# Kernel tuning notes

Hardware: AMD Instinct MI355X
Metric: run time of the kernel (lower is better)

## Reference

```python
import jax, jax.numpy as jnp
import numpy as np


def _gru_dir(x, Wih, Whh, bih, bhh):
    # x: (B,T,I) -> (B,T,H); torch GRU equations, h0 = 0
    H = Whh.shape[1]
    pre = x @ Wih.T + bih  # (B,T,3H), input projection hoisted out of scan
    def step(h, p):
        gh = h @ Whh.T + bhh
        pr, pz, pn = jnp.split(p, 3, axis=-1)
        gr, gz, gn = jnp.split(gh, 3, axis=-1)
        r = jax.nn.sigmoid(pr + gr)
        z = jax.nn.sigmoid(pz + gz)
        n = jnp.tanh(pn + r * gn)
        h = (1.0 - z) * n + z * h
        return h, h
    h0 = jnp.zeros((x.shape[0], H), x.dtype)
    _, ys = jax.lax.scan(step, h0, jnp.swapaxes(pre, 0, 1))
    return jnp.swapaxes(ys, 0, 1)


def _gru_bidir(x, Wih, Whh, bih, bhh):
    f = _gru_dir(x, Wih[0], Whh[0], bih[0], bhh[0])
    b = _gru_dir(x[:, ::-1], Wih[1], Whh[1], bih[1], bhh[1])[:, ::-1]
    return jnp.concatenate([f, b], axis=-1)


def _forward(inputs, embed, l_Wih, l_Whh, l_bih, l_bhh, r_Wih, r_Whh, r_bih, r_bhh,
             a_Wih, a_Whh, a_bih, a_bhh, Wc1, Wc2, vc, Wb, Wd, vd, Wm, vm, Ws, vs,
             Wp, vp, Wpred):
    x = embed[inputs]  # (B,T,E)
    hl = _gru_bidir(x, l_Wih, l_Whh, l_bih, l_bhh)  # (B,T,2H)
    hr = _gru_bidir(x, r_Wih, r_Whh, r_bih, r_bhh)  # (B,T,2H)
    # co-attention: score[b,i,j] = vc . tanh(Wc1 hl_j + Wc2 hr_i)
    s = jnp.tanh((hl @ Wc1.T)[:, None, :, :] + (hr @ Wc2.T)[:, :, None, :])  # (B,T,T,H)
    ptc = jax.nn.softmax((s @ vc.T)[..., 0], axis=-1) @ hl
    # bilinear: hr (Wb hl)^T
    sjt = jnp.einsum('bid,bjd->bij', hr, hl @ Wb.T)
    ptb = jax.nn.softmax(sjt, axis=-1) @ hl
    # multiplicative: vd . tanh(Wd (hl_j * hr_i))
    p = hl[:, None, :, :] * hr[:, :, None, :]  # (B,T,T,2H)
    ptd = jax.nn.softmax((jnp.tanh(p @ Wd.T) @ vd.T)[..., 0], axis=-1) @ hl
    # subtractive: vm . tanh(Wm (hl_j - hr_i))
    d = hl[:, None, :, :] - hr[:, :, None, :]  # (B,T,T,2H)
    ptm = jax.nn.softmax((jnp.tanh(d @ Wm.T) @ vm.T)[..., 0], axis=-1) @ hl
    # self-attention on hr: vs . tanh(Ws (hr_j * hr_i))
    ss = hr[:, None, :, :] * hr[:, :, None, :]  # (B,T,T,2H)
    pts = jax.nn.softmax((jnp.tanh(ss @ Ws.T) @ vs.T)[..., 0], axis=-1) @ hr
    agg = jnp.concatenate([hr, pts, ptc, ptd, ptb, ptm], axis=-1)  # (B,T,12H)
    ar = _gru_bidir(agg, a_Wih, a_Whh, a_bih, a_bhh)  # (B,T,2H)
    # pooling of hl
    sj = jax.nn.softmax(jnp.swapaxes(jnp.tanh(hl @ Wp.T) @ vp.T, 1, 2), axis=-1)  # (B,1,T)
    rl = sj @ hl  # (B,1,2H)
    # final attention over aggregation
    sj2 = jax.nn.softmax(jnp.swapaxes((ar @ Wc1.T + rl @ Wc2.T) @ vc.T, 1, 2), axis=-1)  # (B,1,T)
    rr = (sj2 @ ar)[:, 0, :]  # (B,2H)
    return jax.nn.sigmoid(rr @ Wpred.T)  # (B,labels)


def setup_inputs() -> dict:
    B, T, V, E, H, L = 4, 256, 30000, 300, 128, 2
    key = jax.random.key(0)
    ks = jax.random.split(key, 40)
    inp = {}
    inp['inputs'] = jax.random.randint(ks[0], (B, T), 0, V)
    inp['embed'] = jax.random.uniform(ks[1], (V, E), jnp.float32, -0.1, 0.1)
    ki = 2
    for name, isz in [('l', E), ('r', E), ('a', 12 * H)]:
        inp[name + '_Wih'] = jax.random.normal(ks[ki], (2, 3 * H, isz), jnp.float32) * 0.05; ki += 1
        inp[name + '_Whh'] = jax.random.normal(ks[ki], (2, 3 * H, H), jnp.float32) * 0.05; ki += 1
        inp[name + '_bih'] = jnp.zeros((2, 3 * H), jnp.float32)
        inp[name + '_bhh'] = jnp.zeros((2, 3 * H), jnp.float32)
    for n, o, i in [('Wc1', H, 2 * H), ('Wc2', H, 2 * H), ('vc', 1, H), ('Wb', 2 * H, 2 * H),
                    ('Wd', H, 2 * H), ('vd', 1, H), ('Wm', H, 2 * H), ('vm', 1, H),
                    ('Ws', H, 2 * H), ('vs', 1, H), ('Wp', H, 2 * H), ('vp', 1, H),
                    ('Wpred', L, 2 * H)]:
        inp[n] = jax.random.normal(ks[ki], (o, i), jnp.float32) * 0.05; ki += 1
    return inp


def reference(inputs, embed, l_Wih, l_Whh, l_bih, l_bhh, r_Wih, r_Whh, r_bih, r_bhh,
              a_Wih, a_Whh, a_bih, a_bhh, Wc1, Wc2, vc, Wb, Wd, vd, Wm, vm, Ws, vs,
              Wp, vp, Wpred):
    return _forward(inputs, embed, l_Wih, l_Whh, l_bih, l_bhh, r_Wih, r_Whh, r_bih,
                    r_bhh, a_Wih, a_Whh, a_bih, a_bhh, Wc1, Wc2, vc, Wb, Wd, vd, Wm,
                    vm, Ws, vs, Wp, vp, Wpred)
```

## Files before the change

### kernel.cpp

```cpp
#include <hip/hip_runtime.h>


#define DEV static __device__ __forceinline__
#define BAR_LGKM() __asm__ volatile("s_waitcnt lgkmcnt(0)\ns_barrier" ::: "memory")

typedef __attribute__((ext_vector_type(4))) float f32x4;
typedef __attribute__((ext_vector_type(8))) short s16x8;
typedef __attribute__((ext_vector_type(4))) unsigned int u32x4;
typedef __attribute__((ext_vector_type(2))) unsigned int u32x2;

constexpr int T = 256, E = 300, EP = 320, H = 128, H2 = 256, H3 = 384, H12 = 1536;
constexpr int M = 1024;
constexpr int STY = 262144;

DEV float b2f(unsigned short h) { return __uint_as_float(((unsigned)h) << 16); }
DEV unsigned short f2b(float f) {
  unsigned u = __float_as_uint(f);
  u += 0x7fff + ((u >> 16) & 1);
  return (unsigned short)(u >> 16);
}
DEV unsigned cvt_pk_bf16(float lo, float hi) {
  unsigned r;
  __asm__("v_cvt_pk_bf16_f32 %0, %1, %2" : "=v"(r) : "v"(lo), "v"(hi));
  return r;
}
DEV float rcp_f(float x) {
  float r;
  __asm__("v_rcp_f32 %0, %1" : "=v"(r) : "v"(x));
  return r;
}
DEV float sigm(float x) { return rcp_f(1.f + __expf(-x)); }
DEV float tanh_f(float x) {
  float e = __expf(2.f * x);
  return __builtin_fmaf(-2.f, rcp_f(e + 1.f), 1.f);
}
DEV float plsel(float x0, float x1) {
  u32x2 r = __builtin_amdgcn_permlane32_swap(
      __float_as_uint(x0), __float_as_uint(x1), false, false);
  return __uint_as_float(r[0]);
}

DEV s16x8 ldfrag(const unsigned short* p) {
  u32x4 v = *(const u32x4*)p;
  return __builtin_bit_cast(s16x8, v);
}
DEV f32x4 mfma16(s16x8 a, s16x8 b, f32x4 c) {
  return __builtin_amdgcn_mfma_f32_16x16x32_bf16(a, b, c, 0, 0, 0);
}


struct StageArgs {
  const float* cs[9]; unsigned short* cd[9]; int cn[9];
  const int* idx; const float* emb; unsigned short* xhi; unsigned short* xlo;
  const float* lW; const float* rW; unsigned short* wpad;
  int bo[12];
};

__global__ void k_stage(StageArgs sa) {
  int blk = blockIdx.x;
  int seg = 0;
  #pragma unroll
  for (int s2 = 1; s2 < 11; ++s2) seg = (blk >= sa.bo[s2]) ? s2 : seg;
  int i = (blk - sa.bo[seg]) * 256 + threadIdx.x;
  if (seg < 9) {
    if (i < sa.cn[seg]) sa.cd[seg][i] = f2b(sa.cs[seg][i]);
    return;
  }
  if (seg == 9) {
    if (i >= M * EP) return;
    int m = i / EP, e = i - m * EP;
    int r = sa.idx[m];
    float v = (e < E) ? sa.emb[(size_t)r * E + e] : 0.f;
    unsigned short hi = f2b(v);
    sa.xhi[i] = hi;
    sa.xlo[i] = f2b(v - b2f(hi));
    return;
  }
  if (i >= 4 * H3 * EP) return;
  int e = i % EP, n = (i / EP) % H3, uu = i / (EP * H3);
  const float* src = (uu < 2 ? sa.lW : sa.rW) + (size_t)((uu & 1) * H3 + n) * E;
  sa.wpad[i] = (e < E) ? f2b(src[e]) : (unsigned short)0;
}


struct GemmDesc {
  const unsigned short* Ahi; const unsigned short* Alo; const unsigned short* W;
  const float* bias; float* Cf; int N; int K; int tr;
};
struct GemmBatch { GemmDesc d[8]; };

DEV void gemm_body(const GemmDesc& g, int mb, int nb, int tid) {
  int lane = tid & 63, w = tid >> 6, quad = lane >> 4, l16 = lane & 15;
  int K = g.K;
  const unsigned short* Ahp = g.Ahi + (size_t)(mb + w * 16 + l16) * K + quad * 8;
  const unsigned short* Alp = g.Alo + (size_t)(mb + w * 16 + l16) * K + quad * 8;
  const unsigned short* Wp = g.W + (size_t)(nb + l16) * K + quad * 8;
  f32x4 acc[4];
  #pragma unroll
  for (int nt = 0; nt < 4; ++nt) acc[nt] = f32x4{0.f, 0.f, 0.f, 0.f};
  for (int k = 0; k < K; k += 32) {
    s16x8 ah = ldfrag(Ahp + k);
    s16x8 al = ldfrag(Alp + k);
    #pragma unroll
    for (int nt = 0; nt < 4; ++nt) {
      s16x8 b = ldfrag(Wp + (size_t)nt * 16 * K + k);
      acc[nt] = mfma16(ah, b, acc[nt]);
      acc[nt] = mfma16(al, b, acc[nt]);
    }
  }
  int mr0 = mb + w * 16 + quad * 4;
  #pragma unroll
  for (int nt = 0; nt < 4; ++nt) {
    int col = nb + nt * 16 + l16;
    float bv = g.bias ? g.bias[col] : 0.f;
    #pragma unroll
    for (int r = 0; r < 4; ++r) {
      if (g.tr)
        g.Cf[(size_t)col * M + (mr0 + r)] = acc[nt][r] + bv;
      else
        g.Cf[(size_t)(mr0 + r) * g.N + col] = acc[nt][r] + bv;
    }
  }
}

__global__ __launch_bounds__(256) void k_gemm(GemmBatch gb) {
  GemmDesc g = gb.d[blockIdx.z];
  int nb = blockIdx.y * 64;
  if (nb >= g.N) return;
  gemm_body(g, blockIdx.x * 64, nb, threadIdx.x);
}


struct RecArgs {
  const unsigned short* whh[4];
  const float* pre[4];
  float* outf[4];
  unsigned short* outhi[4];
  unsigned short* outlo[4];
  unsigned short* agghi[4];
  unsigned short* agglo[4];
  const float* bhh[4];
  int colOff[4];
  int dir[4];
};

#define GRU_STEP(pr_, pz_, pn_, pq_, hcur_, hnxt_)                             \
  {                                                                            \
    float pr = pr_, pz = pz_, pn = pn_;                                        \
    pq_ += pst2;                                                               \
    pr_ = pq_[0] + bh_r; pz_ = pq_[128] + bh_z; pn_ = pq_[256];                \
    const unsigned short* hb_ = hcur_ + l16 * 136 + quad * 8;                  \
    s16x8 ah0 = ldfrag(hb_);                                                   \
    s16x8 ah1 = ldfrag(hb_ + 32);                                              \
    s16x8 ah2 = ldfrag(hb_ + 64);                                              \
    s16x8 ah3 = ldfrag(hb_ + 96);                                              \
    f32x4 z4 = f32x4{0.f, 0.f, 0.f, 0.f};                                      \
    f32x4 aR0 = mfma16(ah0, bq[0][0], z4);                                     \
    f32x4 aR1 = mfma16(ah2, bq[0][2], z4);                                     \
    aR0 = mfma16(ah1, bq[0][1], aR0);                                          \
    aR1 = mfma16(ah3, bq[0][3], aR1);                                          \
    f32x4 aZ0 = mfma16(ah0, bq[1][0], z4);                                     \
    f32x4 aZ1 = mfma16(ah2, bq[1][2], z4);                                     \
    aZ0 = mfma16(ah1, bq[1][1], aZ0);                                          \
    aZ1 = mfma16(ah3, bq[1][3], aZ1);                                          \
    float r0 = (aR0[0] + aR1[0]) + (aR0[1] + aR1[1]);                          \
    float r1v = (aR0[2] + aR1[2]) + (aR0[3] + aR1[3]);                         \
    float rg = sigm(pr + plsel(r0, r1v));                                      \
    f32x4 aN0 = mfma16(ah0, bq[2][0], z4);                                     \
    f32x4 aN1 = mfma16(ah2, bq[2][2], z4);                                     \
    aN0 = mfma16(ah1, bq[2][1], aN0);                                          \
    aN1 = mfma16(ah3, bq[2][3], aN1);                                          \
    float z0 = (aZ0[0] + aZ1[0]) + (aZ0[1] + aZ1[1]);                          \
    float z1 = (aZ0[2] + aZ1[2]) + (aZ0[3] + aZ1[3]);                          \
    float zg = sigm(pz + plsel(z0, z1));                                       \
    float n0 = (aN0[0] + aN1[0]) + (aN0[1] + aN1[1]);                          \
    float n1 = (aN0[2] + aN1[2]) + (aN0[3] + aN1[3]);                          \
    float ng = tanh_f(pn + rg * (plsel(n0, n1) + bh_n));                       \
    hf = __builtin_fmaf(zg, hf - ng, ng);                                      \
    unsigned hp32 = cvt_pk_bf16(hf, hf);                                       \
    float rem = hf - __uint_as_float(hp32 << 16);                              \
    unsigned lp32 = cvt_pk_bf16(rem, rem);                                     \
    unsigned short hi = (unsigned short)hp32;                                  \
    unsigned short lo = (unsigned short)lp32;                                  \
    hnxt_[(2 * b) * 136 + d] = hi;                                             \
    hnxt_[(2 * b + 1) * 136 + d] = lo;                                         \
    *outf_p = hf; *outhi_p = hi; *outlo_p = lo;                                \
    outf_p += ost; outhi_p += ost; outlo_p += ost;                             \
    if (agghi_p) { *agghi_p = hi; *agglo_p = lo; agghi_p += ast; agglo_p += ast; } \
    BAR_LGKM();                                                                \
  }

__global__ __launch_bounds__(512) void k_gru(RecArgs ra) {
  int u = blockIdx.x;
  __shared__ __align__(16) unsigned short hs[2][16 * 136];
  int tid = threadIdx.x, lane = tid & 63, w8 = tid >> 6;
  int quad = lane >> 4, l16 = lane & 15;
  for (int i = tid; i < 2 * 16 * 136; i += 512) ((unsigned short*)hs)[i] = 0;
  const unsigned short* whh = ra.whh[u];
  s16x8 bq[3][4];
  #pragma unroll
  for (int g = 0; g < 3; ++g) {
    int row = g * 128 + w8 * 16 + l16;
    #pragma unroll
    for (int kc = 0; kc < 4; ++kc)
      bq[g][kc] = ldfrag(whh + (size_t)row * H + kc * 32 + quad * 8);
  }
  const float* bhh = ra.bhh[u];
  const float* pre = ra.pre[u];
  int colOff = ra.colOff[u], dir = ra.dir[u];
  int b = ((quad & 1) << 1) | (quad >> 1);
  int d = w8 * 16 + l16;
  float bh_r = bhh[d], bh_z = bhh[d + 128], bh_n = bhh[d + 256];
  float hf = 0.f;
  int t0 = dir ? (T - 1) : 0;
  long pst = dir ? -(long)H3 : (long)H3;
  long pst2 = 2 * pst;
  long ost = dir ? -(long)H2 : (long)H2;
  long ast = dir ? -(long)H12 : (long)H12;
  size_t o0 = (size_t)(b * T + t0) * H2 + colOff + d;
  size_t a0 = (size_t)(b * T + t0) * H12 + colOff + d;
  float* outf_p = ra.outf[u] + o0;
  unsigned short* outhi_p = ra.outhi[u] + o0;
  unsigned short* outlo_p = ra.outlo[u] + o0;
  unsigned short* agghi_p = ra.agghi[u] ? ra.agghi[u] + a0 : nullptr;
  unsigned short* agglo_p = ra.agglo[u] ? ra.agglo[u] + a0 : nullptr;
  const float* pqE = pre + (size_t)(b * T + t0) * H3 + d;
  const float* pqO = pqE + pst;
  float e_pr = pqE[0] + bh_r, e_pz = pqE[128] + bh_z, e_pn = pqE[256];
  float o_pr = pqO[0] + bh_r, o_pz = pqO[128] + bh_z, o_pn = pqO[256];
  __syncthreads();
  for (int s = 0; s < T; s += 2) {
    GRU_STEP(e_pr, e_pz, e_pn, pqE, hs[0], hs[1]);
    GRU_STEP(o_pr, o_pz, o_pn, pqO, hs[1], hs[0]);
  }
}


struct ScMMArgs {
  const unsigned short* Xhi[2];
  const float* Rf; const float* Wt[2]; const float* vt[2];
  float* So[2];
};
struct FuseArgs { GemmDesc d[6]; ScMMArgs sm; };

__global__ __launch_bounds__(512, 2) void k_fuse(FuseArgs fa) {
  __shared__ __align__(16) unsigned short w_lds[128 * 256];
  int y = blockIdx.y;
  int tid = threadIdx.x;
  if (y < 6) {
    int xx = blockIdx.x;
    if (xx >= 32) return;
    GemmDesc g = fa.d[y];
    int nb = (xx >> 3) * 64;
    if (nb >= g.N) return;
    int mb = (xx & 7) * 128 + (tid >> 8) * 64;
    gemm_body(g, mb, nb, tid & 255);
    return;
  }
  const ScMMArgs& a = fa.sm;
  int type = y - 6;
  int bi = blockIdx.x, b = bi >> 8;
  const unsigned short* Xhi = a.Xhi[type];
  const float* W = a.Wt[type];
  const float* v = a.vt[type];
  float* Sout = a.So[type];
  int lane = tid & 63, w = tid >> 6, quad = lane >> 4, l16 = lane & 15;
  int d4 = tid & 63, rhi = tid >> 6;
  float4 h4 = ((const float4*)(a.Rf + (size_t)bi * 256))[d4];
  #pragma unroll
  for (int it = 0; it < 16; ++it) {
    int kl = it * 8 + rhi;
    float4 w4 = ((const float4*)(W + (size_t)kl * 256))[d4];
    unsigned lo32 = cvt_pk_bf16(w4.x * h4.x, w4.y * h4.y);
    unsigned hi32 = cvt_pk_bf16(w4.z * h4.z, w4.w * h4.w);
    unsigned long long pk = (unsigned long long)lo32 | ((unsigned long long)hi32 << 32);
    int gphys = ((d4 >> 1) + kl) & 31;
    *(unsigned long long*)(w_lds + (size_t)kl * 256 + gphys * 8 + (d4 & 1) * 4) = pk;
  }
  BAR_LGKM();
  f32x4 acc[2][8];
  #pragma unroll
  for (int jj = 0; jj < 2; ++jj)
    #pragma unroll
    for (int c = 0; c < 8; ++c) acc[jj][c] = f32x4{0.f, 0.f, 0.f, 0.f};
  const unsigned short* Xp0 =
      Xhi + (size_t)(b * 256 + w * 2 * 16 + l16) * 256 + quad * 8;
  #pragma unroll 2
  for (int kc = 0; kc < 8; ++kc) {
    s16x8 bf0 = ldfrag(Xp0 + kc * 32);
    s16x8 bf1 = ldfrag(Xp0 + (size_t)16 * 256 + kc * 32);
    #pragma unroll
    for (int c = 0; c < 8; ++c) {
      int krow = c * 16 + l16;
      int gp = (kc * 4 + quad + krow) & 31;
      s16x8 af = ldfrag(w_lds + (size_t)krow * 256 + gp * 8);
      acc[0][c] = mfma16(af, bf0, acc[0][c]);
      acc[1][c] = mfma16(af, bf1, acc[1][c]);
    }
  }
  #pragma unroll
  for (int jj = 0; jj < 2; ++jj) {
    float s = 0.f;
    #pragma unroll
    for (int c = 0; c < 8; ++c)
      #pragma unroll
      for (int r = 0; r < 4; ++r)
        s += tanh_f(acc[jj][c][r]) * v[c * 16 + quad * 4 + r];
    s += __shfl_xor(s, 16);
    s += __shfl_xor(s, 32);
    int jt = w * 2 + jj;
    if (lane < 16) Sout[(size_t)bi * 256 + jt * 16 + l16] = s;
  }
}


struct ScCmbArgs {
  const float *Hc, *Rc, *Hm, *Rm, *HB, *hrf, *vcf, *vmf; float* S;
};

__global__ __launch_bounds__(256, 2) void k_sccmb(ScCmbArgs a) {
  int bi = blockIdx.x;
  int tid = threadIdx.x;
  __shared__ float rc_l[4 * 128];
  __shared__ float rm_l[4 * 128];
  __shared__ float hr_l[4 * 256];
  __shared__ float vc_l[128], vm_l[128];
  int b = bi >> 6, i0 = (bi & 63) << 2;
  int gi0 = b * 256 + i0;
  {
    const float4* hr4 = (const float4*)(a.hrf + (size_t)gi0 * 256);
    ((float4*)hr_l)[tid] = hr4[tid];
    if (tid < 128) {
      const float4* rc4 = (const float4*)(a.Rc + (size_t)gi0 * 128);
      const float4* rm4 = (const float4*)(a.Rm + (size_t)gi0 * 128);
      ((float4*)rc_l)[tid] = rc4[tid];
      ((float4*)rm_l)[tid] = rm4[tid];
      vc_l[tid] = a.vcf[tid]; vm_l[tid] = a.vmf[tid];
    }
  }
  __syncthreads();
  int j = tid;
  size_t cb = (size_t)(b * 256 + j);
  float scq[4], smq[4], sbq[4];
  #pragma unroll
  for (int q = 0; q < 4; ++q) { scq[q] = 0.f; smq[q] = 0.f; sbq[q] = 0.f; }
  for (int k = 0; k < 128; ++k) {
    float hc = a.Hc[(size_t)k * M + cb];
    float hm = a.Hm[(size_t)k * M + cb];
    float vck = vc_l[k], vmk = vm_l[k];
    #pragma unroll
    for (int q = 0; q < 4; ++q) {
      scq[q] += vck * tanh_f(hc + rc_l[q * 128 + k]);
      smq[q] += vmk * tanh_f(hm - rm_l[q * 128 + k]);
    }
  }
  for (int k = 0; k < 256; ++k) {
    float hb = a.HB[(size_t)k * M + cb];
    #pragma unroll
    for (int q = 0; q < 4; ++q) sbq[q] += hb * hr_l[q * 256 + k];
  }
  #pragma unroll
  for (int q = 0; q < 4; ++q) {
    size_t o = (size_t)(gi0 + q) * 256 + j;
    a.S[(size_t)STY * 1 + o] = scq[q];
    a.S[(size_t)STY * 3 + o] = sbq[q];
    a.S[(size_t)STY * 4 + o] = smq[q];
  }
}


__global__ __launch_bounds__(256) void k_wsum(const float* __restrict__ S,
    const float* __restrict__ hl_f, const float* __restrict__ hr_f,
    unsigned short* __restrict__ ahi, unsigned short* __restrict__ alo) {
  int it = blockIdx.x, type = blockIdx.y, b = blockIdx.z;
  __shared__ float p_l[8][256];
  __shared__ float red[4];
  int tid = threadIdx.x;
  for (int ii = 0; ii < 8; ++ii) {
    size_t idx = ((size_t)(b * 256 + it * 8 + ii)) * 256 + tid;
    float x = S[(size_t)type * STY + idx];
    float m = x;
    for (int dl = 32; dl; dl >>= 1) m = fmaxf(m, __shfl_xor(m, dl));
    if ((tid & 63) == 0) red[tid >> 6] = m;
    __syncthreads();
    m = fmaxf(fmaxf(red[0], red[1]), fmaxf(red[2], red[3]));
    __syncthreads();
    float e = __expf(x - m);
    float sum = e;
    for (int dl = 32; dl; dl >>= 1) sum += __shfl_xor(sum, dl);
    if ((tid & 63) == 0) red[tid >> 6] = sum;
    __syncthreads();
    sum = red[0] + red[1] + red[2] + red[3];
    p_l[ii][tid] = e * rcp_f(sum);
    __syncthreads();
  }
  const float* src = (type == 0 ? hr_f : hl_f) + (size_t)b * 256 * 256;
  float acc[8] = {0.f, 0.f, 0.f, 0.f, 0.f, 0.f, 0.f, 0.f};
  for (int j = 0; j < 256; ++j) {
    float hv = src[(size_t)j * 256 + tid];
    #pragma unroll
    for (int ii = 0; ii < 8; ++ii) acc[ii] += p_l[ii][j] * hv;
  }
  int off = 256 * (1 + type);
  #pragma unroll
  for (int ii = 0; ii < 8; ++ii) {
    float vv = acc[ii];
    unsigned short hi = f2b(vv);
    size_t o = (size_t)(b * 256 + it * 8 + ii) * H12 + off + tid;
    ahi[o] = hi;
    alo[o] = f2b(vv - b2f(hi));
  }
}


__global__ __launch_bounds__(256) void k_tail(const float* __restrict__ Hp,
    const float* __restrict__ hl_f, const float* __restrict__ vpf,
    const float* __restrict__ Wc2f, const float* __restrict__ Arc,
    const float* __restrict__ ar_f, const float* __restrict__ vcf,
    const float* __restrict__ Wpredf, float* __restrict__ out) {
  int b = blockIdx.x, tid = threadIdx.x;
  __shared__ float vl[128], wl[256], rvec[256], rlcl[128], red[4];
  if (tid < 128) vl[tid] = vpf[tid];
  __syncthreads();
  const float* hp = Hp + (size_t)(b * 256 + tid) * 128;
  float s = 0.f;
  for (int k = 0; k < 128; ++k) s += vl[k] * tanh_f(hp[k]);
  float m = s;
  for (int dl = 32; dl; dl >>= 1) m = fmaxf(m, __shfl_xor(m, dl));
  if ((tid & 63) == 0) red[tid >> 6] = m;
  __syncthreads();
  m = fmaxf(fmaxf(red[0], red[1]), fmaxf(red[2], red[3]));
  __syncthreads();
  float e = __expf(s - m);
  float sum = e;
  for (int dl = 32; dl; dl >>= 1) sum += __shfl_xor(sum, dl);
  if ((tid & 63) == 0) red[tid >> 6] = sum;
  __syncthreads();
  sum = red[0] + red[1] + red[2] + red[3];
  wl[tid] = e * rcp_f(sum);
  __syncthreads();
  float acc = 0.f;
  for (int t = 0; t < 256; ++t) acc += wl[t] * hl_f[(size_t)(b * 256 + t) * 256 + tid];
  rvec[tid] = acc;
  __syncthreads();
  if (tid < 128) {
    float a2 = 0.f;
    const float* wr = Wc2f + (size_t)tid * 256;
    for (int dk = 0; dk < 256; ++dk) a2 += rvec[dk] * wr[dk];
    rlcl[tid] = a2;
    vl[tid] = vcf[tid];
  }
  __syncthreads();
  const float* ap = Arc + (size_t)(b * 256 + tid) * 128;
  float s2 = 0.f;
  for (int k = 0; k < 128; ++k) s2 += vl[k] * (ap[k] + rlcl[k]);
  m = s2;
  for (int dl = 32; dl; dl >>= 1) m = fmaxf(m, __shfl_xor(m, dl));
  if ((tid & 63) == 0) red[tid >> 6] = m;
  __syncthreads();
  m = fmaxf(fmaxf(red[0], red[1]), fmaxf(red[2], red[3]));
  __syncthreads();
  float e2 = __expf(s2 - m);
  float sum2 = e2;
  for (int dl = 32; dl; dl >>= 1) sum2 += __shfl_xor(sum2, dl);
  if ((tid & 63) == 0) red[tid >> 6] = sum2;
  __syncthreads();
  sum2 = red[0] + red[1] + red[2] + red[3];
  wl[tid] = e2 * rcp_f(sum2);
  __syncthreads();
  float acc2 = 0.f;
  for (int t = 0; t < 256; ++t) acc2 += wl[t] * ar_f[(size_t)(b * 256 + t) * 256 + tid];
  rvec[tid] = acc2;
  __syncthreads();
  if (tid < 2) {
    float o = 0.f;
    const float* wp = Wpredf + (size_t)tid * 256;
    for (int dk = 0; dk < 256; ++dk) o += rvec[dk] * wp[dk];
    out[b * 2 + tid] = sigm(o);
  }
}


extern "C" void kernel_launch(void* const* d_in, const int* in_sizes, int n_in,
                              void* d_out, int out_size, void* d_ws, size_t ws_size,
                              hipStream_t stream) {
  (void)in_sizes; (void)n_in; (void)out_size; (void)ws_size;
  const int* inputs = (const int*)d_in[0];
  const float* embed = (const float*)d_in[1];
  const float* lWih = (const float*)d_in[2];
  const float* lWhh = (const float*)d_in[3];
  const float* lbih = (const float*)d_in[4];
  const float* lbhh = (const float*)d_in[5];
  const float* rWih = (const float*)d_in[6];
  const float* rWhh = (const float*)d_in[7];
  const float* rbih = (const float*)d_in[8];
  const float* rbhh = (const float*)d_in[9];
  const float* aWih = (const float*)d_in[10];
  const float* aWhh = (const float*)d_in[11];
  const float* abih = (const float*)d_in[12];
  const float* abhh = (const float*)d_in[13];
  const float* Wc1 = (const float*)d_in[14];
  const float* Wc2 = (const float*)d_in[15];
  const float* vc  = (const float*)d_in[16];
  const float* Wb  = (const float*)d_in[17];
  const float* Wd  = (const float*)d_in[18];
  const float* vd  = (const float*)d_in[19];
  const float* Wm  = (const float*)d_in[20];
  const float* vmv = (const float*)d_in[21];
  const float* Wsw = (const float*)d_in[22];
  const float* vsv = (const float*)d_in[23];
  const float* Wp  = (const float*)d_in[24];
  const float* vp  = (const float*)d_in[25];
  const float* Wpred = (const float*)d_in[26];

  char* ws = (char*)d_ws;
  size_t off = 0;
  auto alloc = [&](size_t bytes) -> void* {
    void* p = ws + off;
    off += (bytes + 255) & ~(size_t)255;
    return p;
  };
  unsigned short* xhi = (unsigned short*)alloc((size_t)M * EP * 2);
  unsigned short* xlo = (unsigned short*)alloc((size_t)M * EP * 2);
  unsigned short* wpad = (unsigned short*)alloc((size_t)4 * H3 * EP * 2);
  unsigned short* Whh_b = (unsigned short*)alloc((size_t)6 * H3 * H * 2);
  unsigned short* aWih_b = (unsigned short*)alloc((size_t)2 * H3 * H12 * 2);
  unsigned short* Wc1_b = (unsigned short*)alloc((size_t)H * H2 * 2);
  unsigned short* Wc2_b = (unsigned short*)alloc((size_t)H * H2 * 2);
  unsigned short* Wm_b  = (unsigned short*)alloc((size_t)H * H2 * 2);
  unsigned short* Wp_b  = (unsigned short*)alloc((size_t)H * H2 * 2);
  unsigned short* Wb_b  = (unsigned short*)alloc((size_t)H2 * H2 * 2);
  char* region1 = (char*)alloc((size_t)4 * M * H3 * 4);
  float* pre_lr = (float*)region1;
  float* S      = (float*)region1;
  float* pre_a  = (float*)region1;
  float* hl_f = (float*)alloc((size_t)M * H2 * 4);
  float* hr_f = (float*)alloc((size_t)M * H2 * 4);
  unsigned short* hl_hi = (unsigned short*)alloc((size_t)M * H2 * 2);
  unsigned short* hl_lo = (unsigned short*)alloc((size_t)M * H2 * 2);
  unsigned short* hr_hi = (unsigned short*)alloc((size_t)M * H2 * 2);
  unsigned short* hr_lo = (unsigned short*)alloc((size_t)M * H2 * 2);
  float* Hc = (float*)alloc((size_t)M * H * 4);
  float* Rc = (float*)alloc((size_t)M * H * 4);
  float* Hm = (float*)alloc((size_t)M * H * 4);
  float* Rm = (float*)alloc((size_t)M * H * 4);
  float* Hp = (float*)alloc((size_t)M * H * 4);
  float* HB = (float*)alloc((size_t)M * H2 * 4);
  unsigned short* agg_hi = (unsigned short*)alloc((size_t)M * H12 * 2);
  unsigned short* agg_lo = (unsigned short*)alloc((size_t)M * H12 * 2);
  float* ar_f = (float*)alloc((size_t)M * H2 * 4);
  unsigned short* ar_hi = (unsigned short*)alloc((size_t)M * H2 * 2);
  unsigned short* ar_lo = (unsigned short*)alloc((size_t)M * H2 * 2);
  float* Arc = (float*)alloc((size_t)M * H * 4);

  StageArgs sa{};
  sa.cs[0] = lWhh;  sa.cd[0] = Whh_b;                 sa.cn[0] = 2 * H3 * H;
  sa.cs[1] = rWhh;  sa.cd[1] = Whh_b + 2 * H3 * H;    sa.cn[1] = 2 * H3 * H;
  sa.cs[2] = aWhh;  sa.cd[2] = Whh_b + 4 * H3 * H;    sa.cn[2] = 2 * H3 * H;
  sa.cs[3] = aWih;  sa.cd[3] = aWih_b;                sa.cn[3] = 2 * H3 * H12;
  sa.cs[4] = Wc1;   sa.cd[4] = Wc1_b;                 sa.cn[4] = H * H2;
  sa.cs[5] = Wc2;   sa.cd[5] = Wc2_b;                 sa.cn[5] = H * H2;
  sa.cs[6] = Wm;    sa.cd[6] = Wm_b;                  sa.cn[6] = H * H2;
  sa.cs[7] = Wp;    sa.cd[7] = Wp_b;                  sa.cn[7] = H * H2;
  sa.cs[8] = Wb;    sa.cd[8] = Wb_b;                  sa.cn[8] = H2 * H2;
  sa.idx = inputs; sa.emb = embed; sa.xhi = xhi; sa.xlo = xlo;
  sa.lW = lWih; sa.rW = rWih; sa.wpad = wpad;
  {
    int acc0 = 0;
    sa.bo[0] = 0;
    for (int s = 0; s < 9; ++s) { acc0 += (sa.cn[s] + 255) / 256; sa.bo[s + 1] = acc0; }
    acc0 += (M * EP + 255) / 256;       sa.bo[10] = acc0;
    acc0 += (4 * H3 * EP + 255) / 256;  sa.bo[11] = acc0;
  }
  k_stage<<<dim3(sa.bo[11]), dim3(256), 0, stream>>>(sa);

  GemmBatch ga{};
  const float* biases[4] = { lbih, lbih + H3, rbih, rbih + H3 };
  for (int u = 0; u < 4; ++u)
    ga.d[u] = GemmDesc{ xhi, xlo, wpad + (size_t)u * H3 * EP, biases[u],
                        pre_lr + (size_t)u * M * H3, H3, EP, 0 };
  k_gemm<<<dim3(16, 6, 4), dim3(256), 0, stream>>>(ga);

  RecArgs r1{};
  r1.whh[0] = Whh_b;               r1.whh[1] = Whh_b + H3 * H;
  r1.whh[2] = Whh_b + 2 * H3 * H;  r1.whh[3] = Whh_b + 3 * H3 * H;
  for (int u = 0; u < 4; ++u) r1.pre[u] = pre_lr + (size_t)u * M * H3;
  r1.outf[0] = r1.outf[1] = hl_f; r1.outf[2] = r1.outf[3] = hr_f;
  r1.outhi[0] = r1.outhi[1] = hl_hi; r1.outhi[2] = r1.outhi[3] = hr_hi;
  r1.outlo[0] = r1.outlo[1] = hl_lo; r1.outlo[2] = r1.outlo[3] = hr_lo;
  r1.agghi[0] = r1.agghi[1] = nullptr; r1.agghi[2] = r1.agghi[3] = agg_hi;
  r1.agglo[0] = r1.agglo[1] = nullptr; r1.agglo[2] = r1.agglo[3] = agg_lo;
  r1.bhh[0] = lbhh; r1.bhh[1] = lbhh + H3; r1.bhh[2] = rbhh; r1.bhh[3] = rbhh + H3;
  r1.colOff[0] = 0; r1.colOff[1] = H; r1.colOff[2] = 0; r1.colOff[3] = H;
  r1.dir[0] = 0; r1.dir[1] = 1; r1.dir[2] = 0; r1.dir[3] = 1;
  k_gru<<<dim3(4), dim3(512), 0, stream>>>(r1);

  FuseArgs fu{};
  fu.d[0] = GemmDesc{ hl_hi, hl_lo, Wc1_b, nullptr, Hc, H, H2, 1 };
  fu.d[1] = GemmDesc{ hr_hi, hr_lo, Wc2_b, nullptr, Rc, H, H2, 0 };
  fu.d[2] = GemmDesc{ hl_hi, hl_lo, Wm_b, nullptr, Hm, H, H2, 1 };
  fu.d[3] = GemmDesc{ hr_hi, hr_lo, Wm_b, nullptr, Rm, H, H2, 0 };
  fu.d[4] = GemmDesc{ hl_hi, hl_lo, Wb_b, nullptr, HB, H2, H2, 1 };
  fu.d[5] = GemmDesc{ hl_hi, hl_lo, Wp_b, nullptr, Hp, H, H2, 0 };
  fu.sm.Xhi[0] = hl_hi; fu.sm.Wt[0] = Wd;  fu.sm.vt[0] = vd;
  fu.sm.So[0] = S + (size_t)2 * STY;
  fu.sm.Xhi[1] = hr_hi; fu.sm.Wt[1] = Wsw; fu.sm.vt[1] = vsv;
  fu.sm.So[1] = S + (size_t)0 * STY;
  fu.sm.Rf = hr_f;
  k_fuse<<<dim3(M, 8), dim3(512), 0, stream>>>(fu);

  ScCmbArgs scb{};
  scb.Hc = Hc; scb.Rc = Rc; scb.Hm = Hm; scb.Rm = Rm; scb.HB = HB;
  scb.hrf = hr_f; scb.vcf = vc; scb.vmf = vmv; scb.S = S;
  k_sccmb<<<dim3(256), dim3(256), 0, stream>>>(scb);

  k_wsum<<<dim3(32, 5, 4), dim3(256), 0, stream>>>(S, hl_f, hr_f, agg_hi, agg_lo);

  GemmBatch gc{};
  gc.d[0] = GemmDesc{ agg_hi, agg_lo, aWih_b, abih, pre_a, H3, H12, 0 };
  gc.d[1] = GemmDesc{ agg_hi, agg_lo, aWih_b + (size_t)H3 * H12, abih + H3,
                      pre_a + (size_t)M * H3, H3, H12, 0 };
  k_gemm<<<dim3(16, 6, 2), dim3(256), 0, stream>>>(gc);

  RecArgs r2{};
  r2.whh[0] = Whh_b + 4 * H3 * H; r2.whh[1] = Whh_b + 5 * H3 * H;
  r2.whh[2] = r2.whh[3] = Whh_b + 4 * H3 * H;
  r2.pre[0] = pre_a; r2.pre[1] = pre_a + (size_t)M * H3;
  r2.pre[2] = r2.pre[3] = pre_a;
  r2.outf[0] = r2.outf[1] = r2.outf[2] = r2.outf[3] = ar_f;
  r2.outhi[0] = r2.outhi[1] = r2.outhi[2] = r2.outhi[3] = ar_hi;
  r2.outlo[0] = r2.outlo[1] = r2.outlo[2] = r2.outlo[3] = ar_lo;
  for (int u = 0; u < 4; ++u) { r2.agghi[u] = nullptr; r2.agglo[u] = nullptr; }
  r2.bhh[0] = abhh; r2.bhh[1] = abhh + H3; r2.bhh[2] = r2.bhh[3] = abhh;
  r2.colOff[0] = 0; r2.colOff[1] = H; r2.colOff[2] = r2.colOff[3] = 0;
  r2.dir[0] = 0; r2.dir[1] = 1; r2.dir[2] = r2.dir[3] = 0;
  k_gru<<<dim3(2), dim3(512), 0, stream>>>(r2);

  GemmBatch gd{};
  gd.d[0] = GemmDesc{ ar_hi, ar_lo, Wc1_b, nullptr, Arc, H, H2, 0 };
  k_gemm<<<dim3(16, 2, 1), dim3(256), 0, stream>>>(gd);

  k_tail<<<dim3(4), dim3(256), 0, stream>>>(Hp, hl_f, vp, Wc2, Arc, ar_f, vc, Wpred,
                                            (float*)d_out);
}
```

Before: 658.8 us.

## Overlap side work with serial GRU recurrence blocks and split softmax-sum stages

Several pieces of work move into extra blocks of kernels that are otherwise latency-bound. The first GRU launch now also converts the aggregation and attention weights to bf16, and the second GRU launch also computes the pooled-hl projection that k_tail used to do. The self-attention and multiplicative softmax-weighted sums move from k_wsum into extra blocks of k_sccmb, so they run alongside the score combine. The aim is to fill idle CUs during the 256-step recurrences and shorten the serial k_stage and k_tail. The risk is that the extra blocks contend with the recurrence blocks for memory bandwidth or slow them.

```diff
diff --git a/kernel.cpp b/kernel.cpp
--- a/kernel.cpp
+++ b/kernel.cpp
@@ -50,23 +50,23 @@
 
 
 struct StageArgs {
-  const float* cs[9]; unsigned short* cd[9]; int cn[9];
+  const float* cs[3]; unsigned short* cd[3]; int cn[3];
   const int* idx; const float* emb; unsigned short* xhi; unsigned short* xlo;
   const float* lW; const float* rW; unsigned short* wpad;
-  int bo[12];
+  int bo[6];
 };
 
 __global__ void k_stage(StageArgs sa) {
   int blk = blockIdx.x;
   int seg = 0;
   #pragma unroll
-  for (int s2 = 1; s2 < 11; ++s2) seg = (blk >= sa.bo[s2]) ? s2 : seg;
+  for (int s2 = 1; s2 < 5; ++s2) seg = (blk >= sa.bo[s2]) ? s2 : seg;
   int i = (blk - sa.bo[seg]) * 256 + threadIdx.x;
-  if (seg < 9) {
+  if (seg < 3) {
     if (i < sa.cn[seg]) sa.cd[seg][i] = f2b(sa.cs[seg][i]);
     return;
   }
-  if (seg == 9) {
+  if (seg == 3) {
     if (i >= M * EP) return;
     int m = i / EP, e = i - m * EP;
     int r = sa.idx[m];
@@ -142,6 +142,9 @@
   const float* bhh[4];
   int colOff[4];
   int dir[4];
+  int nGru;
+  const float* ccs[6]; unsigned short* ccd[6]; int ccn[6]; int cbo[7];
+  const float *Hp, *hlf, *vpf, *Wc2f; float* rlcl;
 };
 
 #define GRU_STEP(pr_, pz_, pn_, pq_, hcur_, hnxt_)                             \
@@ -191,9 +194,61 @@
   }
 
 __global__ __launch_bounds__(512) void k_gru(RecArgs ra) {
-  int u = blockIdx.x;
+  int blk = blockIdx.x;
+  int tid = threadIdx.x;
+  if (blk >= ra.nGru) {
+    if (ra.rlcl) {
+      int b = blk - ra.nGru;
+      __shared__ float vl[128], wl[256], rvec[256], red[4];
+      if (tid < 128) vl[tid] = ra.vpf[tid];
+      __syncthreads();
+      float s = 0.f, e = 0.f;
+      if (tid < 256) {
+        const float* hp = ra.Hp + (size_t)(b * 256 + tid) * 128;
+        for (int k = 0; k < 128; ++k) s += vl[k] * tanh_f(hp[k]);
+        float m = s;
+        for (int dl = 32; dl; dl >>= 1) m = fmaxf(m, __shfl_xor(m, dl));
+        if ((tid & 63) == 0) red[tid >> 6] = m;
+      }
+      __syncthreads();
+      float m = fmaxf(fmaxf(red[0], red[1]), fmaxf(red[2], red[3]));
+      __syncthreads();
+      if (tid < 256) {
+        e = __expf(s - m);
+        float sum = e;
+        for (int dl = 32; dl; dl >>= 1) sum += __shfl_xor(sum, dl);
+        if ((tid & 63) == 0) red[tid >> 6] = sum;
+      }
+      __syncthreads();
+      float sum = red[0] + red[1] + red[2] + red[3];
+      if (tid < 256) wl[tid] = e * rcp_f(sum);
+      __syncthreads();
+      if (tid < 256) {
+        float acc = 0.f;
+        for (int t = 0; t < 256; ++t)
+          acc += wl[t] * ra.hlf[(size_t)(b * 256 + t) * 256 + tid];
+        rvec[tid] = acc;
+      }
+      __syncthreads();
+      if (tid < 128) {
+        float a2 = 0.f;
+        const float* wr = ra.Wc2f + (size_t)tid * 256;
+        for (int dk = 0; dk < 256; ++dk) a2 += rvec[dk] * wr[dk];
+        ra.rlcl[b * 128 + tid] = a2;
+      }
+      return;
+    }
+    int cb = blk - ra.nGru;
+    int seg = 0;
+    #pragma unroll
+    for (int s2 = 1; s2 < 6; ++s2) seg = (cb >= ra.cbo[s2]) ? s2 : seg;
+    int i = (cb - ra.cbo[seg]) * 512 + tid;
+    if (i < ra.ccn[seg]) ra.ccd[seg][i] = f2b(ra.ccs[seg][i]);
+    return;
+  }
+  int u = blk;
   __shared__ __align__(16) unsigned short hs[2][16 * 136];
-  int tid = threadIdx.x, lane = tid & 63, w8 = tid >> 6;
+  int lane = tid & 63, w8 = tid >> 6;
   int quad = lane >> 4, l16 = lane & 15;
   for (int i = tid; i < 2 * 16 * 136; i += 512) ((unsigned short*)hs)[i] = 0;
   const unsigned short* whh = ra.whh[u];
@@ -316,11 +371,56 @@
 
 struct ScCmbArgs {
   const float *Hc, *Rc, *Hm, *Rm, *HB, *hrf, *vcf, *vmf; float* S;
+  const float* hlf;
+  unsigned short *ahi, *alo;
 };
 
 __global__ __launch_bounds__(256, 2) void k_sccmb(ScCmbArgs a) {
   int bi = blockIdx.x;
   int tid = threadIdx.x;
+  if (bi >= 256) {
+    int widx = bi - 256;
+    int type = (widx >> 7) * 2;
+    int rem = widx & 127;
+    int it = rem >> 2, b = rem & 3;
+    __shared__ float p_l[8][256];
+    __shared__ float red[4];
+    for (int ii = 0; ii < 8; ++ii) {
+      size_t idx = ((size_t)(b * 256 + it * 8 + ii)) * 256 + tid;
+      float x = a.S[(size_t)type * STY + idx];
+      float m = x;
+      for (int dl = 32; dl; dl >>= 1) m = fmaxf(m, __shfl_xor(m, dl));
+      if ((tid & 63) == 0) red[tid >> 6] = m;
+      __syncthreads();
+      m = fmaxf(fmaxf(red[0], red[1]), fmaxf(red[2], red[3]));
+      __syncthreads();
+      float e = __expf(x - m);
+      float sum = e;
+      for (int dl = 32; dl; dl >>= 1) sum += __shfl_xor(sum, dl);
+      if ((tid & 63) == 0) red[tid >> 6] = sum;
+      __syncthreads();
+      sum = red[0] + red[1] + red[2] + red[3];
+      p_l[ii][tid] = e * rcp_f(sum);
+      __syncthreads();
+    }
+    const float* src = (type == 0 ? a.hrf : a.hlf) + (size_t)b * 256 * 256;
+    float acc[8] = {0.f, 0.f, 0.f, 0.f, 0.f, 0.f, 0.f, 0.f};
+    for (int j = 0; j < 256; ++j) {
+      float hv = src[(size_t)j * 256 + tid];
+      #pragma unroll
+      for (int ii = 0; ii < 8; ++ii) acc[ii] += p_l[ii][j] * hv;
+    }
+    int off = 256 * (1 + type);
+    #pragma unroll
+    for (int ii = 0; ii < 8; ++ii) {
+      float vv = acc[ii];
+      unsigned short hi = f2b(vv);
+      size_t o = (size_t)(b * 256 + it * 8 + ii) * H12 + off + tid;
+      a.ahi[o] = hi;
+      a.alo[o] = f2b(vv - b2f(hi));
+    }
+    return;
+  }
   __shared__ float rc_l[4 * 128];
   __shared__ float rm_l[4 * 128];
   __shared__ float hr_l[4 * 256];
@@ -372,7 +472,9 @@
 __global__ __launch_bounds__(256) void k_wsum(const float* __restrict__ S,
     const float* __restrict__ hl_f, const float* __restrict__ hr_f,
     unsigned short* __restrict__ ahi, unsigned short* __restrict__ alo) {
-  int it = blockIdx.x, type = blockIdx.y, b = blockIdx.z;
+  int it = blockIdx.x, b = blockIdx.z;
+  int y = blockIdx.y;
+  int type = (y == 0) ? 1 : (y + 2);
   __shared__ float p_l[8][256];
   __shared__ float red[4];
   int tid = threadIdx.x;
@@ -394,7 +496,7 @@
     p_l[ii][tid] = e * rcp_f(sum);
     __syncthreads();
   }
-  const float* src = (type == 0 ? hr_f : hl_f) + (size_t)b * 256 * 256;
+  const float* src = hl_f + (size_t)b * 256 * 256;
   float acc[8] = {0.f, 0.f, 0.f, 0.f, 0.f, 0.f, 0.f, 0.f};
   for (int j = 0; j < 256; ++j) {
     float hv = src[(size_t)j * 256 + tid];
@@ -413,48 +515,19 @@
 }
 
 
-__global__ __launch_bounds__(256) void k_tail(const float* __restrict__ Hp,
-    const float* __restrict__ hl_f, const float* __restrict__ vpf,
-    const float* __restrict__ Wc2f, const float* __restrict__ Arc,
-    const float* __restrict__ ar_f, const float* __restrict__ vcf,
-    const float* __restrict__ Wpredf, float* __restrict__ out) {
+__global__ __launch_bounds__(256) void k_tail(const float* __restrict__ rlcl,
+    const float* __restrict__ Arc, const float* __restrict__ ar_f,
+    const float* __restrict__ vcf, const float* __restrict__ Wpredf,
+    float* __restrict__ out) {
   int b = blockIdx.x, tid = threadIdx.x;
-  __shared__ float vl[128], wl[256], rvec[256], rlcl[128], red[4];
-  if (tid < 128) vl[tid] = vpf[tid];
-  __syncthreads();
-  const float* hp = Hp + (size_t)(b * 256 + tid) * 128;
-  float s = 0.f;
-  for (int k = 0; k < 128; ++k) s += vl[k] * tanh_f(hp[k]);
-  float m = s;
-  for (int dl = 32; dl; dl >>= 1) m = fmaxf(m, __shfl_xor(m, dl));
-  if ((tid & 63) == 0) red[tid >> 6] = m;
-  __syncthreads();
-  m = fmaxf(fmaxf(red[0], red[1]), fmaxf(red[2], red[3]));
-  __syncthreads();
-  float e = __expf(s - m);
-  float sum = e;
-  for (int dl = 32; dl; dl >>= 1) sum += __shfl_xor(sum, dl);
-  if ((tid & 63) == 0) red[tid >> 6] = sum;
-  __syncthreads();
-  sum = red[0] + red[1] + red[2] + red[3];
-  wl[tid] = e * rcp_f(sum);
-  __syncthreads();
-  float acc = 0.f;
-  for (int t = 0; t < 256; ++t) acc += wl[t] * hl_f[(size_t)(b * 256 + t) * 256 + tid];
-  rvec[tid] = acc;
-  __syncthreads();
-  if (tid < 128) {
-    float a2 = 0.f;
-    const float* wr = Wc2f + (size_t)tid * 256;
-    for (int dk = 0; dk < 256; ++dk) a2 += rvec[dk] * wr[dk];
-    rlcl[tid] = a2;
-    vl[tid] = vcf[tid];
-  }
+  __shared__ float vl[128], wl[256], rvec[256], red[4];
+  if (tid < 128) vl[tid] = vcf[tid];
   __syncthreads();
   const float* ap = Arc + (size_t)(b * 256 + tid) * 128;
+  const float* rl = rlcl + b * 128;
   float s2 = 0.f;
-  for (int k = 0; k < 128; ++k) s2 += vl[k] * (ap[k] + rlcl[k]);
-  m = s2;
+  for (int k = 0; k < 128; ++k) s2 += vl[k] * (ap[k] + rl[k]);
+  float m = s2;
   for (int dl = 32; dl; dl >>= 1) m = fmaxf(m, __shfl_xor(m, dl));
   if ((tid & 63) == 0) red[tid >> 6] = m;
   __syncthreads();
@@ -552,27 +625,22 @@
   unsigned short* ar_hi = (unsigned short*)alloc((size_t)M * H2 * 2);
   unsigned short* ar_lo = (unsigned short*)alloc((size_t)M * H2 * 2);
   float* Arc = (float*)alloc((size_t)M * H * 4);
+  float* rlcl = (float*)alloc((size_t)4 * H * 4);
 
   StageArgs sa{};
   sa.cs[0] = lWhh;  sa.cd[0] = Whh_b;                 sa.cn[0] = 2 * H3 * H;
   sa.cs[1] = rWhh;  sa.cd[1] = Whh_b + 2 * H3 * H;    sa.cn[1] = 2 * H3 * H;
   sa.cs[2] = aWhh;  sa.cd[2] = Whh_b + 4 * H3 * H;    sa.cn[2] = 2 * H3 * H;
-  sa.cs[3] = aWih;  sa.cd[3] = aWih_b;                sa.cn[3] = 2 * H3 * H12;
-  sa.cs[4] = Wc1;   sa.cd[4] = Wc1_b;                 sa.cn[4] = H * H2;
-  sa.cs[5] = Wc2;   sa.cd[5] = Wc2_b;                 sa.cn[5] = H * H2;
-  sa.cs[6] = Wm;    sa.cd[6] = Wm_b;                  sa.cn[6] = H * H2;
-  sa.cs[7] = Wp;    sa.cd[7] = Wp_b;                  sa.cn[7] = H * H2;
-  sa.cs[8] = Wb;    sa.cd[8] = Wb_b;                  sa.cn[8] = H2 * H2;
   sa.idx = inputs; sa.emb = embed; sa.xhi = xhi; sa.xlo = xlo;
   sa.lW = lWih; sa.rW = rWih; sa.wpad = wpad;
   {
     int acc0 = 0;
     sa.bo[0] = 0;
-    for (int s = 0; s < 9; ++s) { acc0 += (sa.cn[s] + 255) / 256; sa.bo[s + 1] = acc0; }
-    acc0 += (M * EP + 255) / 256;       sa.bo[10] = acc0;
-    acc0 += (4 * H3 * EP + 255) / 256;  sa.bo[11] = acc0;
-  }
-  k_stage<<<dim3(sa.bo[11]), dim3(256), 0, stream>>>(sa);
+    for (int s = 0; s < 3; ++s) { acc0 += (sa.cn[s] + 255) / 256; sa.bo[s + 1] = acc0; }
+    acc0 += (M * EP + 255) / 256;       sa.bo[4] = acc0;
+    acc0 += (4 * H3 * EP + 255) / 256;  sa.bo[5] = acc0;
+  }
+  k_stage<<<dim3(sa.bo[5]), dim3(256), 0, stream>>>(sa);
 
   GemmBatch ga{};
   const float* biases[4] = { lbih, lbih + H3, rbih, rbih + H3 };
@@ -593,7 +661,23 @@
   r1.bhh[0] = lbhh; r1.bhh[1] = lbhh + H3; r1.bhh[2] = rbhh; r1.bhh[3] = rbhh + H3;
   r1.colOff[0] = 0; r1.colOff[1] = H; r1.colOff[2] = 0; r1.colOff[3] = H;
   r1.dir[0] = 0; r1.dir[1] = 1; r1.dir[2] = 0; r1.dir[3] = 1;
-  k_gru<<<dim3(4), dim3(512), 0, stream>>>(r1);
+  r1.nGru = 4;
+  r1.ccs[0] = aWih; r1.ccd[0] = aWih_b; r1.ccn[0] = 2 * H3 * H12;
+  r1.ccs[1] = Wc1;  r1.ccd[1] = Wc1_b;  r1.ccn[1] = H * H2;
+  r1.ccs[2] = Wc2;  r1.ccd[2] = Wc2_b;  r1.ccn[2] = H * H2;
+  r1.ccs[3] = Wm;   r1.ccd[3] = Wm_b;   r1.ccn[3] = H * H2;
+  r1.ccs[4] = Wp;   r1.ccd[4] = Wp_b;   r1.ccn[4] = H * H2;
+  r1.ccs[5] = Wb;   r1.ccd[5] = Wb_b;   r1.ccn[5] = H2 * H2;
+  int cvtBlocks;
+  {
+    int acc0 = 0;
+    r1.cbo[0] = 0;
+    for (int s = 0; s < 6; ++s) { acc0 += (r1.ccn[s] + 511) / 512; r1.cbo[s + 1] = acc0; }
+    cvtBlocks = acc0;
+  }
+  r1.Hp = nullptr; r1.hlf = nullptr; r1.vpf = nullptr; r1.Wc2f = nullptr;
+  r1.rlcl = nullptr;
+  k_gru<<<dim3(4 + cvtBlocks), dim3(512), 0, stream>>>(r1);
 
   FuseArgs fu{};
   fu.d[0] = GemmDesc{ hl_hi, hl_lo, Wc1_b, nullptr, Hc, H, H2, 1 };
@@ -612,9 +696,10 @@
   ScCmbArgs scb{};
   scb.Hc = Hc; scb.Rc = Rc; scb.Hm = Hm; scb.Rm = Rm; scb.HB = HB;
   scb.hrf = hr_f; scb.vcf = vc; scb.vmf = vmv; scb.S = S;
-  k_sccmb<<<dim3(256), dim3(256), 0, stream>>>(scb);
-
-  k_wsum<<<dim3(32, 5, 4), dim3(256), 0, stream>>>(S, hl_f, hr_f, agg_hi, agg_lo);
+  scb.hlf = hl_f; scb.ahi = agg_hi; scb.alo = agg_lo;
+  k_sccmb<<<dim3(512), dim3(256), 0, stream>>>(scb);
+
+  k_wsum<<<dim3(32, 3, 4), dim3(256), 0, stream>>>(S, hl_f, hr_f, agg_hi, agg_lo);
 
   GemmBatch gc{};
   gc.d[0] = GemmDesc{ agg_hi, agg_lo, aWih_b, abih, pre_a, H3, H12, 0 };
@@ -634,12 +719,16 @@
   r2.bhh[0] = abhh; r2.bhh[1] = abhh + H3; r2.bhh[2] = r2.bhh[3] = abhh;
   r2.colOff[0] = 0; r2.colOff[1] = H; r2.colOff[2] = r2.colOff[3] = 0;
   r2.dir[0] = 0; r2.dir[1] = 1; r2.dir[2] = r2.dir[3] = 0;
-  k_gru<<<dim3(2), dim3(512), 0, stream>>>(r2);
+  r2.nGru = 2;
+  for (int s = 0; s < 6; ++s) { r2.ccs[s] = nullptr; r2.ccd[s] = nullptr; r2.ccn[s] = 0; }
+  for (int s = 0; s < 7; ++s) r2.cbo[s] = 0;
+  r2.Hp = Hp; r2.hlf = hl_f; r2.vpf = vp; r2.Wc2f = Wc2; r2.rlcl = rlcl;
+  k_gru<<<dim3(2 + 4), dim3(512), 0, stream>>>(r2);
 
   GemmBatch gd{};
   gd.d[0] = GemmDesc{ ar_hi, ar_lo, Wc1_b, nullptr, Arc, H, H2, 0 };
   k_gemm<<<dim3(16, 2, 1), dim3(256), 0, stream>>>(gd);
 
-  k_tail<<<dim3(4), dim3(256), 0, stream>>>(Hp, hl_f, vp, Wc2, Arc, ar_f, vc, Wpred,
+  k_tail<<<dim3(4), dim3(256), 0, stream>>>(rlcl, Arc, ar_f, vc, Wpred,
                                             (float*)d_out);
 }
```

Measured after the change: 628.1 us. 4.7% less time.
